# Performance work log

Measured on AMD Instinct MI355X. Metric: run time of the kernel, lower is better.

Reference implementation:

```python
import jax, jax.numpy as jnp
import numpy as np

N_NODES = 100000
N_EDGES = 600000
IN_C = 128


def setup_inputs() -> dict:
    key = jax.random.key(0)
    ks = jax.random.split(key, 10)
    x = jax.random.normal(ks[0], (N_NODES, IN_C), dtype=jnp.float32)
    edge_index = jax.random.randint(ks[1], (2, N_EDGES), 0, N_NODES, dtype=jnp.int64)
    edge_weight = jax.random.uniform(ks[2], (N_EDGES,), dtype=jnp.float32)
    s = 1.0 / np.sqrt(IN_C)
    # EvolveGCNO initial GCN weight [in, in]
    W0 = jax.random.uniform(ks[3], (IN_C, IN_C), minval=-s, maxval=s, dtype=jnp.float32)
    # GRU(input=in, hidden=in) params, gate order (r, z, n)
    W_ih = jax.random.uniform(ks[4], (3 * IN_C, IN_C), minval=-s, maxval=s, dtype=jnp.float32)
    W_hh = jax.random.uniform(ks[5], (3 * IN_C, IN_C), minval=-s, maxval=s, dtype=jnp.float32)
    b_ih = jax.random.uniform(ks[6], (3 * IN_C,), minval=-s, maxval=s, dtype=jnp.float32)
    b_hh = jax.random.uniform(ks[7], (3 * IN_C,), minval=-s, maxval=s, dtype=jnp.float32)
    cls_w = jax.random.uniform(ks[8], (1, IN_C), minval=-s, maxval=s, dtype=jnp.float32)
    cls_b = jax.random.uniform(ks[9], (1,), minval=-s, maxval=s, dtype=jnp.float32)
    return {"x": x, "edge_index": edge_index, "edge_weight": edge_weight,
            "W0": W0, "W_ih": W_ih, "W_hh": W_hh, "b_ih": b_ih, "b_hh": b_hh,
            "cls_w": cls_w, "cls_b": cls_b}


def reference(x, edge_index, edge_weight, W0, W_ih, W_hh, b_ih, b_hh, cls_w, cls_b):
    n = x.shape[0]
    # --- EvolveGCNO: GRU step with input = hidden = W0 (batch = in_channels rows) ---
    gi = W0 @ W_ih.T + b_ih
    gh = W0 @ W_hh.T + b_hh
    i_r, i_z, i_n = jnp.split(gi, 3, axis=1)
    h_r, h_z, h_n = jnp.split(gh, 3, axis=1)
    r = jax.nn.sigmoid(i_r + h_r)
    z = jax.nn.sigmoid(i_z + h_z)
    cand = jnp.tanh(i_n + r * h_n)
    W = (1.0 - z) * cand + z * W0  # evolved GCN weight [in, in]
    # --- GCNConv with fixed W: add self-loops, symmetric normalization ---
    loops = jnp.arange(n, dtype=edge_index.dtype)
    row = jnp.concatenate([edge_index[0], loops])  # source
    col = jnp.concatenate([edge_index[1], loops])  # target
    w = jnp.concatenate([edge_weight, jnp.ones((n,), x.dtype)])
    deg = jax.ops.segment_sum(w, col, num_segments=n)
    dinv = jnp.where(deg > 0, jax.lax.rsqrt(jnp.maximum(deg, 1e-30)), 0.0)
    norm = dinv[row] * w * dinv[col]  # [E+N]
    h = x @ W  # [N, in]
    agg = jax.ops.segment_sum(norm[:, None] * h[row], col, num_segments=n)  # [N, in]
    # --- ReLU + linear classifier ---
    h = jax.nn.relu(agg)
    return h @ cls_w.T + cls_b  # [N, 1]
```

## Files before the change

### kernel.cpp

```cpp
#include <hip/hip_runtime.h>
#include <math.h>

#define IN_C 128

typedef short short8 __attribute__((ext_vector_type(8)));
typedef float floatx4 __attribute__((ext_vector_type(4)));

static __device__ __forceinline__ unsigned short f2bf(float f) {
    unsigned int u = __float_as_uint(f);
    u += 0x7fffu + ((u >> 16) & 1u);
    return (unsigned short)(u >> 16);
}

__global__ void evolve_w(const float* __restrict__ W0,
                         const float* __restrict__ Wih,
                         const float* __restrict__ Whh,
                         const float* __restrict__ bih,
                         const float* __restrict__ bhh,
                         unsigned short* __restrict__ Wbt) {
    __shared__ float w0row[IN_C];
    const int i = blockIdx.x;
    const int j = threadIdx.x;
    w0row[j] = W0[i * IN_C + j];
    __syncthreads();

    float ir = bih[j], iz = bih[j + IN_C], inn = bih[j + 2 * IN_C];
    float hr = bhh[j], hz = bhh[j + IN_C], hnn = bhh[j + 2 * IN_C];
    const float* wr = &Wih[(size_t)j * IN_C];
    const float* wz = &Wih[(size_t)(j + IN_C) * IN_C];
    const float* wn = &Wih[(size_t)(j + 2 * IN_C) * IN_C];
    const float* ur = &Whh[(size_t)j * IN_C];
    const float* uz = &Whh[(size_t)(j + IN_C) * IN_C];
    const float* un = &Whh[(size_t)(j + 2 * IN_C) * IN_C];
    #pragma unroll 4
    for (int k = 0; k < IN_C; ++k) {
        const float a = w0row[k];
        ir = fmaf(a, wr[k], ir); iz = fmaf(a, wz[k], iz); inn = fmaf(a, wn[k], inn);
        hr = fmaf(a, ur[k], hr); hz = fmaf(a, uz[k], hz); hnn = fmaf(a, un[k], hnn);
    }
    const float r = 1.0f / (1.0f + expf(-(ir + hr)));
    const float z = 1.0f / (1.0f + expf(-(iz + hz)));
    const float cand = tanhf(inn + r * hnn);
    Wbt[j * IN_C + i] = f2bf((1.0f - z) * cand + z * w0row[j]);
}

__global__ __launch_bounds__(256) void hist_rank(const int* __restrict__ coli,
                                                 const float* __restrict__ ew,
                                                 unsigned long long* __restrict__ pk,
                                                 unsigned int* __restrict__ rank, int E) {
    const int e0 = (blockIdx.x * 256 + threadIdx.x) * 4;
    if (e0 + 3 < E) {
        const int4 c4 = *(const int4*)&coli[e0];
        const float4 w4 = *(const float4*)&ew[e0];
        const unsigned long long o0 = atomicAdd(&pk[c4.x], (1ull << 32) | (unsigned long long)(unsigned int)(w4.x * 16777216.0f));
        const unsigned long long o1 = atomicAdd(&pk[c4.y], (1ull << 32) | (unsigned long long)(unsigned int)(w4.y * 16777216.0f));
        const unsigned long long o2 = atomicAdd(&pk[c4.z], (1ull << 32) | (unsigned long long)(unsigned int)(w4.z * 16777216.0f));
        const unsigned long long o3 = atomicAdd(&pk[c4.w], (1ull << 32) | (unsigned long long)(unsigned int)(w4.w * 16777216.0f));
        uint4 rk;
        rk.x = (unsigned int)(o0 >> 32); rk.y = (unsigned int)(o1 >> 32);
        rk.z = (unsigned int)(o2 >> 32); rk.w = (unsigned int)(o3 >> 32);
        *(uint4*)&rank[e0] = rk;
    } else {
        for (int e = e0; e < E; ++e) {
            const unsigned long long o = atomicAdd(&pk[coli[e]],
                (1ull << 32) | (unsigned long long)(unsigned int)(ew[e] * 16777216.0f));
            rank[e] = (unsigned int)(o >> 32);
        }
    }
}

__global__ void scan1(const unsigned long long* __restrict__ pk, int* __restrict__ rowptr,
                      int* __restrict__ partials, float* __restrict__ dinv, int n) {
    __shared__ int s[256];
    const int t = threadIdx.x;
    const int i = blockIdx.x * 256 + t;
    const unsigned long long pv = (i < n) ? pk[i] : 0ull;
    if (i < n)
        dinv[i] = rsqrtf((float)(unsigned int)(pv & 0xffffffffull) * (1.0f / 16777216.0f) + 1.0f);
    s[t] = (int)(pv >> 32);
    __syncthreads();
    #pragma unroll
    for (int off = 1; off < 256; off <<= 1) {
        const int v = (t >= off) ? s[t - off] : 0;
        __syncthreads();
        s[t] += v;
        __syncthreads();
    }
    if (i < n) rowptr[i] = (t == 0) ? 0 : s[t - 1];
    if (t == 255) partials[blockIdx.x] = s[255];
}

__global__ void scan2(int* __restrict__ partials, int* __restrict__ rowptr, int nb, int n, int E) {
    __shared__ int s[512];
    const int t = threadIdx.x;
    s[t] = (t < nb) ? partials[t] : 0;
    __syncthreads();
    #pragma unroll
    for (int off = 1; off < 512; off <<= 1) {
        const int v = (t >= off) ? s[t - off] : 0;
        __syncthreads();
        s[t] += v;
        __syncthreads();
    }
    if (t < nb) partials[t] = (t == 0) ? 0 : s[t - 1];
    if (t == 0) rowptr[n] = E;
}

__global__ void scan3(int* __restrict__ rowptr, const int* __restrict__ partials, int n) {
    const int i = blockIdx.x * blockDim.x + threadIdx.x;
    if (i < n) rowptr[i] += partials[blockIdx.x];
}

__global__ __launch_bounds__(256) void place(const int* __restrict__ rowi,
                                             const int* __restrict__ coli,
                                             const float* __restrict__ ew,
                                             const float* __restrict__ dinv,
                                             const int* __restrict__ rowptr,
                                             const unsigned int* __restrict__ rank,
                                             uint2* __restrict__ edge_sn, int E) {
    const int e0 = (blockIdx.x * 256 + threadIdx.x) * 4;
    if (e0 + 3 < E) {
        const int4 r4 = *(const int4*)&rowi[e0];
        const int4 c4 = *(const int4*)&coli[e0];
        const float4 w4 = *(const float4*)&ew[e0];
        const uint4 rk = *(const uint4*)&rank[e0];
        edge_sn[rowptr[c4.x] + rk.x] = make_uint2((unsigned)r4.x, __float_as_uint(dinv[r4.x] * w4.x * dinv[c4.x]));
        edge_sn[rowptr[c4.y] + rk.y] = make_uint2((unsigned)r4.y, __float_as_uint(dinv[r4.y] * w4.y * dinv[c4.y]));
        edge_sn[rowptr[c4.z] + rk.z] = make_uint2((unsigned)r4.z, __float_as_uint(dinv[r4.z] * w4.z * dinv[c4.z]));
        edge_sn[rowptr[c4.w] + rk.w] = make_uint2((unsigned)r4.w, __float_as_uint(dinv[r4.w] * w4.w * dinv[c4.w]));
    } else {
        for (int e = e0; e < E; ++e) {
            const int r = rowi[e], c = coli[e];
            edge_sn[rowptr[c] + rank[e]] = make_uint2((unsigned)r, __float_as_uint(dinv[r] * ew[e] * dinv[c]));
        }
    }
}

#define ALD 136
__global__ __launch_bounds__(256) void gemm_bf16(const float* __restrict__ x,
                                                 const unsigned short* __restrict__ Wbt,
                                                 unsigned short* __restrict__ hb, int n) {
    __shared__ unsigned short As[128 * ALD];
    __shared__ unsigned short Ws[128 * ALD];
    const int t = threadIdx.x;
    const size_t row0 = (size_t)blockIdx.x * 128;

    for (int idx = t; idx < 2048; idx += 256) {
        const int nn = idx >> 4, k8 = (idx & 15) * 8;
        *(uint4*)&Ws[nn * ALD + k8] = *(const uint4*)&Wbt[nn * IN_C + k8];
    }
    for (int idx = t; idx < 4096; idx += 256) {
        const int r = idx >> 5, c4 = (idx & 31) * 4;
        size_t row = row0 + r;
        if (row >= (size_t)n) row = (size_t)n - 1;
        const float4 v = *(const float4*)&x[row * IN_C + c4];
        ushort4 bb;
        bb.x = f2bf(v.x); bb.y = f2bf(v.y); bb.z = f2bf(v.z); bb.w = f2bf(v.w);
        *(ushort4*)&As[r * ALD + c4] = bb;
    }
    __syncthreads();

    const int w = t >> 6, lane = t & 63, ln = lane & 15, quad = lane >> 4;
    floatx4 acc[2][8];
    #pragma unroll
    for (int mt = 0; mt < 2; ++mt)
        #pragma unroll
        for (int nt = 0; nt < 8; ++nt)
            acc[mt][nt] = (floatx4){0.f, 0.f, 0.f, 0.f};

    #pragma unroll
    for (int k0 = 0; k0 < 128; k0 += 32) {
        const short8 a0 = *(const short8*)&As[(w * 32 + ln) * ALD + k0 + quad * 8];
        const short8 a1 = *(const short8*)&As[(w * 32 + 16 + ln) * ALD + k0 + quad * 8];
        #pragma unroll
        for (int nt = 0; nt < 8; ++nt) {
            const short8 bb = *(const short8*)&Ws[(nt * 16 + ln) * ALD + k0 + quad * 8];
            acc[0][nt] = __builtin_amdgcn_mfma_f32_16x16x32_bf16(a0, bb, acc[0][nt], 0, 0, 0);
            acc[1][nt] = __builtin_amdgcn_mfma_f32_16x16x32_bf16(a1, bb, acc[1][nt], 0, 0, 0);
        }
    }

    #pragma unroll
    for (int mt = 0; mt < 2; ++mt) {
        #pragma unroll
        for (int reg = 0; reg < 4; ++reg) {
            const size_t row = row0 + w * 32 + mt * 16 + quad * 4 + reg;
            if (row < (size_t)n) {
                #pragma unroll
                for (int nt = 0; nt < 8; ++nt)
                    hb[row * IN_C + nt * 16 + ln] = f2bf(acc[mt][nt][reg]);
            }
        }
    }
}

__global__ __launch_bounds__(256) void gather_classify(
        const unsigned short* __restrict__ hb, const float* __restrict__ dinv,
        const int* __restrict__ rowptr, const uint2* __restrict__ edge_sn,
        const float* __restrict__ cls_w, const float* __restrict__ cls_b,
        float* __restrict__ out, int n) {
    const int wid = __builtin_amdgcn_readfirstlane((blockIdx.x * blockDim.x + threadIdx.x) >> 6);
    const int lane = threadIdx.x & 63;
    if (wid >= n) return;

    const float dv = dinv[wid];
    unsigned int hv = *(const unsigned int*)&hb[(size_t)wid * IN_C + 2 * lane];
    float ax = dv * dv * __uint_as_float(hv << 16);
    float ay = dv * dv * __uint_as_float(hv & 0xffff0000u);

    const int e0 = rowptr[wid];
    const int e1 = rowptr[wid + 1];
    const int e1m1 = e1 - 1;
    for (int e = e0; e < e1; e += 8) {
        uint2 p[8];
        #pragma unroll
        for (int i = 0; i < 8; ++i) {
            const int idx = (e + i < e1) ? (e + i) : e1m1;
            p[i] = edge_sn[idx];
        }
        unsigned int hr[8];
        #pragma unroll
        for (int i = 0; i < 8; ++i)
            hr[i] = *(const unsigned int*)&hb[(size_t)p[i].x * IN_C + 2 * lane];
        #pragma unroll
        for (int i = 0; i < 8; ++i) {
            const float nm = (e + i < e1) ? __uint_as_float(p[i].y) : 0.0f;
            ax = fmaf(nm, __uint_as_float(hr[i] << 16), ax);
            ay = fmaf(nm, __uint_as_float(hr[i] & 0xffff0000u), ay);
        }
    }

    const float2 wv = *(const float2*)&cls_w[2 * lane];
    float sum = wv.x * fmaxf(ax, 0.0f) + wv.y * fmaxf(ay, 0.0f);
    #pragma unroll
    for (int off = 32; off > 0; off >>= 1) sum += __shfl_down(sum, off);
    if (lane == 0) out[wid] = sum + cls_b[0];
}

extern "C" void kernel_launch(void* const* d_in, const int* in_sizes, int n_in,
                              void* d_out, int out_size, void* d_ws, size_t ws_size,
                              hipStream_t stream) {
    const float* x    = (const float*)d_in[0];
    const int*   eidx = (const int*)d_in[1];
    const float* ew   = (const float*)d_in[2];
    const float* W0   = (const float*)d_in[3];
    const float* Wih  = (const float*)d_in[4];
    const float* Whh  = (const float*)d_in[5];
    const float* bih  = (const float*)d_in[6];
    const float* bhh  = (const float*)d_in[7];
    const float* clsw = (const float*)d_in[8];
    const float* clsb = (const float*)d_in[9];
    float* out = (float*)d_out;

    const int n = in_sizes[0] / IN_C;
    const int E = in_sizes[2];
    const int* rowi = eidx;
    const int* coli = eidx + E;
    const int NB = (n + 255) / 256;

    int* base = (int*)d_ws;
    unsigned long long* pk = (unsigned long long*)base;
    float* dinv   = (float*)(base + 2 * (size_t)n);
    int* rowptr   = base + 3 * (size_t)n;
    int* partials = base + 4 * (size_t)n + 4;
    unsigned int* rank = (unsigned int*)(base + 4 * (size_t)n + 516);
    size_t off = 4 * (size_t)n + 516 + (size_t)E;
    uint2* edge_sn = (uint2*)(base + off);
    unsigned short* Wbt = (unsigned short*)(base + off + 2 * (size_t)E);
    unsigned short* hb  = Wbt + 16384;

    const int EB = (E + 1023) / 1024;

    evolve_w<<<dim3(IN_C), dim3(IN_C), 0, stream>>>(W0, Wih, Whh, bih, bhh, Wbt);
    hipMemsetAsync(pk, 0, (size_t)n * 8, stream);
    hist_rank<<<dim3(EB), dim3(256), 0, stream>>>(coli, ew, pk, rank, E);
    scan1<<<dim3(NB), dim3(256), 0, stream>>>(pk, rowptr, partials, dinv, n);
    scan2<<<dim3(1), dim3(512), 0, stream>>>(partials, rowptr, NB, n, E);
    scan3<<<dim3(NB), dim3(256), 0, stream>>>(rowptr, partials, n);
    place<<<dim3(EB), dim3(256), 0, stream>>>(rowi, coli, ew, dinv, rowptr, rank, edge_sn, E);
    gemm_bf16<<<dim3((n + 127) / 128), dim3(256), 0, stream>>>(x, Wbt, hb, n);
    gather_classify<<<dim3((n + 3) / 4), dim3(256), 0, stream>>>(hb, dinv, rowptr, edge_sn,
                                                                 clsw, clsb, out, n);
}
```

Before: 223.4 us.

## Merge independent stages into fewer kernel launches via block-range dispatch

Fuses evolve_w with hist_rank into one launch, and place with the bf16 GEMM, each split by block-index ranges so the independent stages run together in a single grid. It also merges scan2 and scan3 so every block redundantly scans the partials and applies its own offset. Edge records become packed u64 values written and read with nontemporal hints. The aim is to cut launch gaps and let the small serial stages overlap. The cost is larger shared-memory blocks for the place half of the grid and a redundant partials scan in every block.

```diff
diff --git a/kernel.cpp b/kernel.cpp
--- a/kernel.cpp
+++ b/kernel.cpp
@@ -5,6 +5,7 @@
 
 typedef short short8 __attribute__((ext_vector_type(8)));
 typedef float floatx4 __attribute__((ext_vector_type(4)));
+typedef unsigned long long u64;
 
 static __device__ __forceinline__ unsigned short f2bf(float f) {
     unsigned int u = __float_as_uint(f);
@@ -12,69 +13,73 @@
     return (unsigned short)(u >> 16);
 }
 
-__global__ void evolve_w(const float* __restrict__ W0,
-                         const float* __restrict__ Wih,
-                         const float* __restrict__ Whh,
-                         const float* __restrict__ bih,
-                         const float* __restrict__ bhh,
-                         unsigned short* __restrict__ Wbt) {
-    __shared__ float w0row[IN_C];
-    const int i = blockIdx.x;
-    const int j = threadIdx.x;
-    w0row[j] = W0[i * IN_C + j];
-    __syncthreads();
-
-    float ir = bih[j], iz = bih[j + IN_C], inn = bih[j + 2 * IN_C];
-    float hr = bhh[j], hz = bhh[j + IN_C], hnn = bhh[j + 2 * IN_C];
-    const float* wr = &Wih[(size_t)j * IN_C];
-    const float* wz = &Wih[(size_t)(j + IN_C) * IN_C];
-    const float* wn = &Wih[(size_t)(j + 2 * IN_C) * IN_C];
-    const float* ur = &Whh[(size_t)j * IN_C];
-    const float* uz = &Whh[(size_t)(j + IN_C) * IN_C];
-    const float* un = &Whh[(size_t)(j + 2 * IN_C) * IN_C];
-    #pragma unroll 4
-    for (int k = 0; k < IN_C; ++k) {
-        const float a = w0row[k];
-        ir = fmaf(a, wr[k], ir); iz = fmaf(a, wz[k], iz); inn = fmaf(a, wn[k], inn);
-        hr = fmaf(a, ur[k], hr); hz = fmaf(a, uz[k], hz); hnn = fmaf(a, un[k], hnn);
-    }
-    const float r = 1.0f / (1.0f + expf(-(ir + hr)));
-    const float z = 1.0f / (1.0f + expf(-(iz + hz)));
-    const float cand = tanhf(inn + r * hnn);
-    Wbt[j * IN_C + i] = f2bf((1.0f - z) * cand + z * w0row[j]);
-}
-
-__global__ __launch_bounds__(256) void hist_rank(const int* __restrict__ coli,
-                                                 const float* __restrict__ ew,
-                                                 unsigned long long* __restrict__ pk,
-                                                 unsigned int* __restrict__ rank, int E) {
-    const int e0 = (blockIdx.x * 256 + threadIdx.x) * 4;
-    if (e0 + 3 < E) {
-        const int4 c4 = *(const int4*)&coli[e0];
-        const float4 w4 = *(const float4*)&ew[e0];
-        const unsigned long long o0 = atomicAdd(&pk[c4.x], (1ull << 32) | (unsigned long long)(unsigned int)(w4.x * 16777216.0f));
-        const unsigned long long o1 = atomicAdd(&pk[c4.y], (1ull << 32) | (unsigned long long)(unsigned int)(w4.y * 16777216.0f));
-        const unsigned long long o2 = atomicAdd(&pk[c4.z], (1ull << 32) | (unsigned long long)(unsigned int)(w4.z * 16777216.0f));
-        const unsigned long long o3 = atomicAdd(&pk[c4.w], (1ull << 32) | (unsigned long long)(unsigned int)(w4.w * 16777216.0f));
-        uint4 rk;
-        rk.x = (unsigned int)(o0 >> 32); rk.y = (unsigned int)(o1 >> 32);
-        rk.z = (unsigned int)(o2 >> 32); rk.w = (unsigned int)(o3 >> 32);
-        *(uint4*)&rank[e0] = rk;
+static __device__ __forceinline__ u64 pack_sn(unsigned int src, float norm) {
+    return (u64)src | ((u64)__float_as_uint(norm) << 32);
+}
+
+__global__ __launch_bounds__(256) void evolve_hist(
+        const float* __restrict__ W0, const float* __restrict__ Wih,
+        const float* __restrict__ Whh, const float* __restrict__ bih,
+        const float* __restrict__ bhh, unsigned short* __restrict__ Wbt,
+        const int* __restrict__ coli, const float* __restrict__ ew,
+        u64* __restrict__ pk, unsigned int* __restrict__ rank, int E) {
+    const int b = blockIdx.x;
+    const int t = threadIdx.x;
+
+    if (b < 64) {
+        __shared__ float w0row[2][IN_C];
+        const int r2 = t >> 7;
+        const int j = t & 127;
+        const int i = b * 2 + r2;
+        w0row[r2][j] = W0[i * IN_C + j];
+        __syncthreads();
+        float ir = bih[j], iz = bih[j + IN_C], inn = bih[j + 2 * IN_C];
+        float hr = bhh[j], hz = bhh[j + IN_C], hnn = bhh[j + 2 * IN_C];
+        const float* wr = &Wih[(size_t)j * IN_C];
+        const float* wz = &Wih[(size_t)(j + IN_C) * IN_C];
+        const float* wn = &Wih[(size_t)(j + 2 * IN_C) * IN_C];
+        const float* ur = &Whh[(size_t)j * IN_C];
+        const float* uz = &Whh[(size_t)(j + IN_C) * IN_C];
+        const float* un = &Whh[(size_t)(j + 2 * IN_C) * IN_C];
+        #pragma unroll 4
+        for (int k = 0; k < IN_C; ++k) {
+            const float a = w0row[r2][k];
+            ir = fmaf(a, wr[k], ir); iz = fmaf(a, wz[k], iz); inn = fmaf(a, wn[k], inn);
+            hr = fmaf(a, ur[k], hr); hz = fmaf(a, uz[k], hz); hnn = fmaf(a, un[k], hnn);
+        }
+        const float r = 1.0f / (1.0f + expf(-(ir + hr)));
+        const float z = 1.0f / (1.0f + expf(-(iz + hz)));
+        const float cand = tanhf(inn + r * hnn);
+        Wbt[j * IN_C + i] = f2bf((1.0f - z) * cand + z * w0row[r2][j]);
     } else {
-        for (int e = e0; e < E; ++e) {
-            const unsigned long long o = atomicAdd(&pk[coli[e]],
-                (1ull << 32) | (unsigned long long)(unsigned int)(ew[e] * 16777216.0f));
-            rank[e] = (unsigned int)(o >> 32);
-        }
-    }
-}
-
-__global__ void scan1(const unsigned long long* __restrict__ pk, int* __restrict__ rowptr,
+        const int e0 = ((b - 64) * 256 + t) * 4;
+        if (e0 + 3 < E) {
+            const int4 c4 = *(const int4*)&coli[e0];
+            const float4 w4 = *(const float4*)&ew[e0];
+            const u64 o0 = atomicAdd(&pk[c4.x], (1ull << 32) | (u64)(unsigned int)(w4.x * 16777216.0f));
+            const u64 o1 = atomicAdd(&pk[c4.y], (1ull << 32) | (u64)(unsigned int)(w4.y * 16777216.0f));
+            const u64 o2 = atomicAdd(&pk[c4.z], (1ull << 32) | (u64)(unsigned int)(w4.z * 16777216.0f));
+            const u64 o3 = atomicAdd(&pk[c4.w], (1ull << 32) | (u64)(unsigned int)(w4.w * 16777216.0f));
+            uint4 rk;
+            rk.x = (unsigned int)(o0 >> 32); rk.y = (unsigned int)(o1 >> 32);
+            rk.z = (unsigned int)(o2 >> 32); rk.w = (unsigned int)(o3 >> 32);
+            *(uint4*)&rank[e0] = rk;
+        } else {
+            for (int e = e0; e < E; ++e) {
+                const u64 o = atomicAdd(&pk[coli[e]],
+                    (1ull << 32) | (u64)(unsigned int)(ew[e] * 16777216.0f));
+                rank[e] = (unsigned int)(o >> 32);
+            }
+        }
+    }
+}
+
+__global__ void scan1(const u64* __restrict__ pk, int* __restrict__ rowptr,
                       int* __restrict__ partials, float* __restrict__ dinv, int n) {
     __shared__ int s[256];
     const int t = threadIdx.x;
     const int i = blockIdx.x * 256 + t;
-    const unsigned long long pv = (i < n) ? pk[i] : 0ull;
+    const u64 pv = (i < n) ? pk[i] : 0ull;
     if (i < n)
         dinv[i] = rsqrtf((float)(unsigned int)(pv & 0xffffffffull) * (1.0f / 16777216.0f) + 1.0f);
     s[t] = (int)(pv >> 32);
@@ -90,9 +95,12 @@
     if (t == 255) partials[blockIdx.x] = s[255];
 }
 
-__global__ void scan2(int* __restrict__ partials, int* __restrict__ rowptr, int nb, int n, int E) {
+__global__ __launch_bounds__(512) void scan23(int* __restrict__ rowptr,
+                                              const int* __restrict__ partials,
+                                              int nb, int n, int E) {
     __shared__ int s[512];
     const int t = threadIdx.x;
+    const int b = blockIdx.x;
     s[t] = (t < nb) ? partials[t] : 0;
     __syncthreads();
     #pragma unroll
@@ -102,48 +110,48 @@
         s[t] += v;
         __syncthreads();
     }
-    if (t < nb) partials[t] = (t == 0) ? 0 : s[t - 1];
-    if (t == 0) rowptr[n] = E;
-}
-
-__global__ void scan3(int* __restrict__ rowptr, const int* __restrict__ partials, int n) {
-    const int i = blockIdx.x * blockDim.x + threadIdx.x;
-    if (i < n) rowptr[i] += partials[blockIdx.x];
-}
-
-__global__ __launch_bounds__(256) void place(const int* __restrict__ rowi,
-                                             const int* __restrict__ coli,
-                                             const float* __restrict__ ew,
-                                             const float* __restrict__ dinv,
-                                             const int* __restrict__ rowptr,
-                                             const unsigned int* __restrict__ rank,
-                                             uint2* __restrict__ edge_sn, int E) {
-    const int e0 = (blockIdx.x * 256 + threadIdx.x) * 4;
-    if (e0 + 3 < E) {
-        const int4 r4 = *(const int4*)&rowi[e0];
-        const int4 c4 = *(const int4*)&coli[e0];
-        const float4 w4 = *(const float4*)&ew[e0];
-        const uint4 rk = *(const uint4*)&rank[e0];
-        edge_sn[rowptr[c4.x] + rk.x] = make_uint2((unsigned)r4.x, __float_as_uint(dinv[r4.x] * w4.x * dinv[c4.x]));
-        edge_sn[rowptr[c4.y] + rk.y] = make_uint2((unsigned)r4.y, __float_as_uint(dinv[r4.y] * w4.y * dinv[c4.y]));
-        edge_sn[rowptr[c4.z] + rk.z] = make_uint2((unsigned)r4.z, __float_as_uint(dinv[r4.z] * w4.z * dinv[c4.z]));
-        edge_sn[rowptr[c4.w] + rk.w] = make_uint2((unsigned)r4.w, __float_as_uint(dinv[r4.w] * w4.w * dinv[c4.w]));
-    } else {
-        for (int e = e0; e < E; ++e) {
-            const int r = rowi[e], c = coli[e];
-            edge_sn[rowptr[c] + rank[e]] = make_uint2((unsigned)r, __float_as_uint(dinv[r] * ew[e] * dinv[c]));
-        }
-    }
+    const int add = (b == 0) ? 0 : s[b - 1];
+    if (t < 256) {
+        const int i = b * 256 + t;
+        if (i < n) rowptr[i] += add;
+    }
+    if (b == 0 && t == 0) rowptr[n] = E;
 }
 
 #define ALD 136
-__global__ __launch_bounds__(256) void gemm_bf16(const float* __restrict__ x,
-                                                 const unsigned short* __restrict__ Wbt,
-                                                 unsigned short* __restrict__ hb, int n) {
+__global__ __launch_bounds__(256) void place_gemm(
+        const int* __restrict__ rowi, const int* __restrict__ coli,
+        const float* __restrict__ ew, const float* __restrict__ dinv,
+        const int* __restrict__ rowptr, const unsigned int* __restrict__ rank,
+        u64* __restrict__ edge_sn, int E, int PB,
+        const float* __restrict__ x, const unsigned short* __restrict__ Wbt,
+        unsigned short* __restrict__ hb, int n) {
     __shared__ unsigned short As[128 * ALD];
     __shared__ unsigned short Ws[128 * ALD];
-    const int t = threadIdx.x;
-    const size_t row0 = (size_t)blockIdx.x * 128;
+    const int b = blockIdx.x;
+    const int t = threadIdx.x;
+
+    if (b < PB) {
+        const int e0 = (b * 256 + t) * 4;
+        if (e0 + 3 < E) {
+            const int4 r4 = *(const int4*)&rowi[e0];
+            const int4 c4 = *(const int4*)&coli[e0];
+            const float4 w4 = *(const float4*)&ew[e0];
+            const uint4 rk = *(const uint4*)&rank[e0];
+            __builtin_nontemporal_store(pack_sn((unsigned)r4.x, dinv[r4.x] * w4.x * dinv[c4.x]), &edge_sn[rowptr[c4.x] + rk.x]);
+            __builtin_nontemporal_store(pack_sn((unsigned)r4.y, dinv[r4.y] * w4.y * dinv[c4.y]), &edge_sn[rowptr[c4.y] + rk.y]);
+            __builtin_nontemporal_store(pack_sn((unsigned)r4.z, dinv[r4.z] * w4.z * dinv[c4.z]), &edge_sn[rowptr[c4.z] + rk.z]);
+            __builtin_nontemporal_store(pack_sn((unsigned)r4.w, dinv[r4.w] * w4.w * dinv[c4.w]), &edge_sn[rowptr[c4.w] + rk.w]);
+        } else {
+            for (int e = e0; e < E; ++e) {
+                const int r = rowi[e], c = coli[e];
+                edge_sn[rowptr[c] + rank[e]] = pack_sn((unsigned)r, dinv[r] * ew[e] * dinv[c]);
+            }
+        }
+        return;
+    }
+
+    const size_t row0 = (size_t)(b - PB) * 128;
 
     for (int idx = t; idx < 2048; idx += 256) {
         const int nn = idx >> 4, k8 = (idx & 15) * 8;
@@ -196,7 +204,7 @@
 
 __global__ __launch_bounds__(256) void gather_classify(
         const unsigned short* __restrict__ hb, const float* __restrict__ dinv,
-        const int* __restrict__ rowptr, const uint2* __restrict__ edge_sn,
+        const int* __restrict__ rowptr, const u64* __restrict__ edge_sn,
         const float* __restrict__ cls_w, const float* __restrict__ cls_b,
         float* __restrict__ out, int n) {
     const int wid = __builtin_amdgcn_readfirstlane((blockIdx.x * blockDim.x + threadIdx.x) >> 6);
@@ -212,19 +220,19 @@
     const int e1 = rowptr[wid + 1];
     const int e1m1 = e1 - 1;
     for (int e = e0; e < e1; e += 8) {
-        uint2 p[8];
+        u64 p[8];
         #pragma unroll
         for (int i = 0; i < 8; ++i) {
             const int idx = (e + i < e1) ? (e + i) : e1m1;
-            p[i] = edge_sn[idx];
+            p[i] = __builtin_nontemporal_load(&edge_sn[idx]);
         }
         unsigned int hr[8];
         #pragma unroll
         for (int i = 0; i < 8; ++i)
-            hr[i] = *(const unsigned int*)&hb[(size_t)p[i].x * IN_C + 2 * lane];
+            hr[i] = *(const unsigned int*)&hb[(size_t)(unsigned int)(p[i] & 0xffffffffull) * IN_C + 2 * lane];
         #pragma unroll
         for (int i = 0; i < 8; ++i) {
-            const float nm = (e + i < e1) ? __uint_as_float(p[i].y) : 0.0f;
+            const float nm = (e + i < e1) ? __uint_as_float((unsigned int)(p[i] >> 32)) : 0.0f;
             ax = fmaf(nm, __uint_as_float(hr[i] << 16), ax);
             ay = fmaf(nm, __uint_as_float(hr[i] & 0xffff0000u), ay);
         }
@@ -259,26 +267,26 @@
     const int NB = (n + 255) / 256;
 
     int* base = (int*)d_ws;
-    unsigned long long* pk = (unsigned long long*)base;
+    u64* pk = (u64*)base;
     float* dinv   = (float*)(base + 2 * (size_t)n);
     int* rowptr   = base + 3 * (size_t)n;
     int* partials = base + 4 * (size_t)n + 4;
     unsigned int* rank = (unsigned int*)(base + 4 * (size_t)n + 516);
     size_t off = 4 * (size_t)n + 516 + (size_t)E;
-    uint2* edge_sn = (uint2*)(base + off);
+    u64* edge_sn = (u64*)(base + off);
     unsigned short* Wbt = (unsigned short*)(base + off + 2 * (size_t)E);
     unsigned short* hb  = Wbt + 16384;
 
     const int EB = (E + 1023) / 1024;
-
-    evolve_w<<<dim3(IN_C), dim3(IN_C), 0, stream>>>(W0, Wih, Whh, bih, bhh, Wbt);
-    hipMemsetAsync(pk, 0, (size_t)n * 8, stream);
-    hist_rank<<<dim3(EB), dim3(256), 0, stream>>>(coli, ew, pk, rank, E);
+    const int GB = (n + 127) / 128;
+
+    (void)hipMemsetAsync(pk, 0, (size_t)n * 8, stream);
+    evolve_hist<<<dim3(64 + EB), dim3(256), 0, stream>>>(W0, Wih, Whh, bih, bhh, Wbt,
+                                                         coli, ew, pk, rank, E);
     scan1<<<dim3(NB), dim3(256), 0, stream>>>(pk, rowptr, partials, dinv, n);
-    scan2<<<dim3(1), dim3(512), 0, stream>>>(partials, rowptr, NB, n, E);
-    scan3<<<dim3(NB), dim3(256), 0, stream>>>(rowptr, partials, n);
-    place<<<dim3(EB), dim3(256), 0, stream>>>(rowi, coli, ew, dinv, rowptr, rank, edge_sn, E);
-    gemm_bf16<<<dim3((n + 127) / 128), dim3(256), 0, stream>>>(x, Wbt, hb, n);
+    scan23<<<dim3(NB), dim3(512), 0, stream>>>(rowptr, partials, NB, n, E);
+    place_gemm<<<dim3(EB + GB), dim3(256), 0, stream>>>(rowi, coli, ew, dinv, rowptr, rank,
+                                                        edge_sn, E, EB, x, Wbt, hb, n);
     gather_classify<<<dim3((n + 3) / 4), dim3(256), 0, stream>>>(hb, dinv, rowptr, edge_sn,
                                                                  clsw, clsb, out, n);
 }
```

New measurement: 229.0 us. 1.03x slower.
